# Performance work log

Hardware: AMD Instinct MI355X
Metric: run time of the kernel (lower is better)

The kernel has to match this reference:

```python
import jax, jax.numpy as jnp
import numpy as np

HEADS = 8
VTH = 1.0
TAU = 2.0          # spikingjelly LIFNode default tau
RS = 64            # region size for bi-level routing
TOPK = 4           # routed regions per query region
ALPHA = 2.0        # ATan surrogate alpha


@jax.custom_vjp
def spike(x):
    # Heaviside forward, ATan surrogate backward (spikingjelly surrogate.ATan)
    return (x >= 0.0).astype(x.dtype)

def _spike_fwd(x):
    return spike(x), x

def _spike_bwd(x, g):
    return (g * (ALPHA / 2.0) / (1.0 + (jnp.pi / 2.0 * ALPHA * x) ** 2),)

spike.defvjp(_spike_fwd, _spike_bwd)


def lif(x):
    # x: [Lt, b, L, dim]; multi-step LIF, v_reset=0 hard reset, detach_reset=True
    def step(v, xt):
        v = v + (xt - v) / TAU
        s = spike(v - VTH)
        v = v * (1.0 - jax.lax.stop_gradient(s))
        return v, s
    _, s = jax.lax.scan(step, jnp.zeros_like(x[0]), x)
    return s


def batchnorm(x, gamma, beta, eps=1e-5):
    # BatchNorm1d(dim) applied to [Lt*b, dim, L]: stats over (Lt, b, L) per channel
    mean = x.mean(axis=(0, 1, 2), keepdims=True)
    var = x.var(axis=(0, 1, 2), keepdims=True)
    return (x - mean) * jax.lax.rsqrt(var + eps) * gamma + beta


def bilevel_attn(s, Wqkv, bqkv, Wo, bo):
    Lt, b, L, dim = s.shape
    R = L // RS
    hd = dim // HEADS
    q, k, v = jnp.split(s @ Wqkv + bqkv, 3, axis=-1)            # each [Lt,b,L,dim]
    # coarse region-level routing on mean-pooled q/k
    qr = q.reshape(Lt, b, R, RS, dim).mean(3)                    # [Lt,b,R,dim]
    kr = k.reshape(Lt, b, R, RS, dim).mean(3)
    aff = jnp.einsum('tbrd,tbsd->tbrs', qr, kr)                  # [Lt,b,R,R]
    _, idx = jax.lax.top_k(aff, TOPK)                            # [Lt,b,R,TOPK]
    kreg = k.reshape(Lt, b, R, RS, HEADS, hd)
    vreg = v.reshape(Lt, b, R, RS, HEADS, hd)
    gidx = idx[:, :, :, :, None, None, None]
    kg = jnp.take_along_axis(kreg[:, :, None], gidx, axis=3).reshape(Lt, b, R, TOPK * RS, HEADS, hd)
    vg = jnp.take_along_axis(vreg[:, :, None], gidx, axis=3).reshape(Lt, b, R, TOPK * RS, HEADS, hd)
    qt = q.reshape(Lt, b, R, RS, HEADS, hd)
    scores = jnp.einsum('tbrihd,tbrjhd->tbrhij', qt, kg) / np.sqrt(hd).astype(np.float32)
    p = jax.nn.softmax(scores, axis=-1)
    out = jnp.einsum('tbrhij,tbrjhd->tbrihd', p, vg).reshape(Lt, b, L, dim)
    return out @ Wo + bo


def _block(x, bn1_gamma, bn1_beta, Wqkv, bqkv, Wo, bo,
           bn2_gamma, bn2_beta, W1, b1, W2, b2, scale):
    s1 = lif(batchnorm(x, bn1_gamma, bn1_beta))
    x = x + bilevel_attn(s1, Wqkv, bqkv, Wo, bo) * scale
    s2 = lif(batchnorm(x, bn2_gamma, bn2_beta))
    h = jax.nn.gelu(s2 @ W1 + b1, approximate=False)
    x = x + (h @ W2 + b2) * scale
    return x


def setup_inputs() -> dict:
    key = jax.random.key(0)
    ks = jax.random.split(key, 8)
    Lt, b, L, dim = 4, 8, 1024, 256
    x = jax.random.normal(ks[0], (Lt, b, L, dim), dtype=jnp.float32)
    w = lambda k, sh: 0.02 * jax.random.normal(k, sh, dtype=jnp.float32)
    return {
        'x': x,
        'bn1_gamma': jnp.ones((dim,), jnp.float32),
        'bn1_beta': jnp.zeros((dim,), jnp.float32),
        'Wqkv': w(ks[1], (dim, 3 * dim)),
        'bqkv': jnp.zeros((3 * dim,), jnp.float32),
        'Wo': w(ks[2], (dim, dim)),
        'bo': jnp.zeros((dim,), jnp.float32),
        'bn2_gamma': jnp.ones((dim,), jnp.float32),
        'bn2_beta': jnp.zeros((dim,), jnp.float32),
        'W1': w(ks[3], (dim, 4 * dim)),
        'b1': jnp.zeros((4 * dim,), jnp.float32),
        'W2': w(ks[4], (4 * dim, dim)),
        'b2': jnp.zeros((dim,), jnp.float32),
        'scale': jnp.array(0.5, jnp.float32),
        'Lt': Lt, 'b': b, 'L': L, 'dim': dim,
    }


def reference(x, bn1_gamma, bn1_beta, Wqkv, bqkv, Wo, bo,
              bn2_gamma, bn2_beta, W1, b1, W2, b2, scale,
              Lt, b, L, dim):
    return _block(x, bn1_gamma, bn1_beta, Wqkv, bqkv, Wo, bo,
                  bn2_gamma, bn2_beta, W1, b1, W2, b2, scale)
```

## Files before the change

kernel.cpp:

```cpp
#include <hip/hip_runtime.h>
#include <hip/hip_bf16.h>
#include <math.h>

typedef __hip_bfloat16 bf16;
typedef unsigned long long u64;
typedef unsigned int u32;

#define LTT 4
#define DIM 256
#define NTOK 32768
#define MT 2097152
#define NTOT 8388608

typedef __attribute__((ext_vector_type(8))) short short8;
typedef __attribute__((ext_vector_type(4))) float f32x4;
typedef __attribute__((ext_vector_type(4))) u32 u32x4;

__device__ __forceinline__ float ldin(const void* p, size_t i, int f) {
  float v = f ? ((const float*)p)[i] : __bfloat162float(((const bf16*)p)[i]);
  return isfinite(v) ? v : 0.0f;
}

__device__ __forceinline__ short bf16bits(float x) {
  union { bf16 b; short s; } u; u.b = __float2bfloat16(x); return u.s;
}

struct PtrPack { const void* p[14]; int n[14]; };

__global__ void probe_all_k(PtrPack pk, int* flags) {
  int b = blockIdx.x;
  int tid = threadIdx.x;
  const unsigned short* u = (const unsigned short*)pk.p[b];
  int nelem = pk.n[b];
  int n = nelem < 1024 ? nelem : 1024;
  bool big = false, nz = false;
  for (int i = tid; i < n; i += 64) {
    unsigned short h = u[i];
    if (((h >> 7) & 0xFF) >= 0xC0) big = true;
    if (h != 0) nz = true;
  }
  u64 bm = __ballot(big);
  u64 zm = __ballot(nz);
  if (tid == 0) {
    unsigned short h0 = u[0];
    int f = 0;
    if (bm != 0ull) f = 1;
    else if (h0 == 0 && (zm != 0ull || n == 1)) f = 1;
    flags[b] = f;
    if (b == 0) flags[15] = 1;
  }
}

__global__ void bnstats_k(const void* __restrict__ x, const int* __restrict__ fxp,
                          float* __restrict__ gsum, float* __restrict__ gsq) {
  int fx = *fxp;
  int c = threadIdx.x;
  int tok0 = blockIdx.x * 128;
  float s = 0.f, q = 0.f;
  for (int t = 0; t < 128; t++) {
    float v = ldin(x, (size_t)(tok0 + t) * DIM + c, fx);
    s += v; q += v * v;
  }
  atomicAdd(&gsum[c], s);
  atomicAdd(&gsq[c], q);
}

__global__ void lif_k(const void* __restrict__ x, const int* __restrict__ fxp,
                      const float* __restrict__ gsum, const float* __restrict__ gsq,
                      const void* __restrict__ gamma, const int* __restrict__ fgp,
                      const void* __restrict__ beta, const int* __restrict__ fbp,
                      u64* __restrict__ bits) {
  int fx = *fxp, fg = *fgp, fb = *fbp;
  int m = blockIdx.x * 256 + threadIdx.x;
  int c = m & (DIM - 1);
  int lane = threadIdx.x & 63;
  float mean = gsum[c] * (1.0f / 32768.0f);
  float var  = gsq[c] * (1.0f / 32768.0f) - mean * mean;
  float inv  = rsqrtf(var + 1e-5f);
  float g = ldin(gamma, c, fg), be = ldin(beta, c, fb);
  float v = 0.f;
  #pragma unroll
  for (int t = 0; t < LTT; t++) {
    size_t e = (size_t)t * MT + m;
    float xn = (ldin(x, e, fx) - mean) * inv * g + be;
    v = v + (xn - v) * 0.5f;
    bool sp = (v - 1.0f >= 0.0f);
    u64 bl = __ballot(sp);
    if (lane == 0) bits[e >> 6] = bl;
    v = sp ? 0.0f : v;
  }
}

__device__ __forceinline__ float gelu_f(float x) {
  return 0.5f * x * (1.0f + erff(x * 0.70710678118654752440f));
}

__global__ void wconv_all_k(const void* __restrict__ Wqkv, const void* __restrict__ Wo,
                            const void* __restrict__ W1, const void* __restrict__ W2,
                            const int* __restrict__ flags,
                            bf16* __restrict__ wqkvt, bf16* __restrict__ wot,
                            bf16* __restrict__ w1t, bf16* __restrict__ w2t) {
  int b = blockIdx.x, t = threadIdx.x;
  const void* W; const int* f; bf16* o; int K, N, n, kblk = 0;
  if (b < 768)       { W = Wqkv; f = flags + 3;  o = wqkvt; K = 256;  N = 768;  n = b; }
  else if (b < 1024) { W = Wo;   f = flags + 5;  o = wot;   K = 256;  N = 256;  n = b - 768; }
  else if (b < 2048) { W = W1;   f = flags + 9;  o = w1t;   K = 256;  N = 1024; n = b - 1024; }
  else { W = W2; f = flags + 11; o = w2t; K = 1024; N = 256;
         int q = b - 2048; kblk = q >> 8; n = q & 255; }
  int k = kblk * 256 + t;
  o[(size_t)n * K + k] = __float2bfloat16(ldin(W, (size_t)k * N + n, *f));
}

template <int MODE, int ABITS>
__global__ void __launch_bounds__(256)
dgemm_k(const void* __restrict__ Av, const bf16* __restrict__ Bt,
        const void* __restrict__ biasv, const int* __restrict__ fbp,
        void* O, const void* xinv, const int* __restrict__ fxp,
        const void* __restrict__ scalev, const int* __restrict__ fsp,
        int N, int K, size_t obase) {
  int tid = threadIdx.x;
  int lane = tid & 63, w = tid >> 6;
  int wr = w >> 1, wc = w & 1;
  int kq = lane >> 4, lr = lane & 15;
  int bm = blockIdx.y * 128, bn = blockIdx.x * 128;
  f32x4 acc[4][4] = {};

  if constexpr (ABITS) {
    __shared__ __align__(16) short lut[256][8];
    {
      short8 e;
      #pragma unroll
      for (int j = 0; j < 8; j++) e[j] = ((tid >> j) & 1) ? (short)0x3F80 : (short)0;
      *(short8*)&lut[tid][0] = e;
    }
    const u32* Abits = (const u32*)Av;
    u32 ab[4][8];
    #pragma unroll
    for (int i = 0; i < 4; i++) {
      const u32* rp = &Abits[(size_t)(bm + wr * 64 + i * 16 + lr) * 8];
      *(u32x4*)&ab[i][0] = *(const u32x4*)&rp[0];
      *(u32x4*)&ab[i][4] = *(const u32x4*)&rp[4];
    }
    __syncthreads();
    #pragma unroll
    for (int s = 0; s < 8; s++) {
      short8 af[4], bf[4];
      #pragma unroll
      for (int i = 0; i < 4; i++) {
        u32 byte = (ab[i][s] >> (kq * 8)) & 0xFFu;
        af[i] = *(const short8*)&lut[byte][0];
      }
      #pragma unroll
      for (int j = 0; j < 4; j++)
        bf[j] = *(const short8*)&Bt[(size_t)(bn + wc * 64 + j * 16 + lr) * 256 + s * 32 + kq * 8];
      #pragma unroll
      for (int i = 0; i < 4; i++)
        #pragma unroll
        for (int j = 0; j < 4; j++)
          acc[i][j] = __builtin_amdgcn_mfma_f32_16x16x32_bf16(af[i], bf[j], acc[i][j], 0, 0, 0);
    }
  } else {
    const bf16* Ab = (const bf16*)Av;
    for (int k0 = 0; k0 < K; k0 += 32) {
      short8 af[4], bf[4];
      #pragma unroll
      for (int i = 0; i < 4; i++)
        af[i] = *(const short8*)&Ab[(size_t)(bm + wr * 64 + i * 16 + lr) * K + k0 + kq * 8];
      #pragma unroll
      for (int j = 0; j < 4; j++)
        bf[j] = *(const short8*)&Bt[(size_t)(bn + wc * 64 + j * 16 + lr) * K + k0 + kq * 8];
      #pragma unroll
      for (int i = 0; i < 4; i++)
        #pragma unroll
        for (int j = 0; j < 4; j++)
          acc[i][j] = __builtin_amdgcn_mfma_f32_16x16x32_bf16(af[i], bf[j], acc[i][j], 0, 0, 0);
    }
  }

  float scl = 0.f;
  int fx = 0, fbias = *fbp;
  if (MODE == 4) { scl = ldin(scalev, 0, *fsp); fx = *fxp; }
  int row0 = bm + wr * 64 + kq * 4;
  int col0 = bn + wc * 64 + lr;
  #pragma unroll
  for (int j = 0; j < 4; j++) {
    int n = col0 + j * 16;
    float bb = ldin(biasv, n, fbias);
    #pragma unroll
    for (int i = 0; i < 4; i++) {
      #pragma unroll
      for (int r = 0; r < 4; r++) {
        int m = row0 + i * 16 + r;
        float v = acc[i][j][r] + bb;
        size_t o = obase + (size_t)m * N + n;
        if (MODE == 2) {
          ((bf16*)O)[o] = __float2bfloat16(gelu_f(v));
        } else if (MODE == 3) {
          ((bf16*)O)[o] = __float2bfloat16(v);
        } else {
          float base = ldin(xinv, o, fx);
          ((float*)O)[o] = base + scl * v;
        }
      }
    }
  }
}

__global__ void __launch_bounds__(256)
ffn_k(const u64* __restrict__ bits_, const bf16* __restrict__ w1t,
      const void* __restrict__ b1v, const int* __restrict__ f1p,
      const bf16* __restrict__ w2t,
      const void* __restrict__ b2v, const int* __restrict__ f2p,
      float* out, const void* __restrict__ scalev, const int* __restrict__ fsp) {
  __shared__ __align__(16) short lut[256][8];
  __shared__ __align__(16) short hlds[16][64][8];
  int tid = threadIdx.x;
  int lane = tid & 63, w = tid >> 6;
  int kq = lane >> 4, lr = lane & 15;
  int m0 = blockIdx.x * 64;
  {
    short8 e;
    #pragma unroll
    for (int j = 0; j < 8; j++) e[j] = ((tid >> j) & 1) ? (short)0x3F80 : (short)0;
    *(short8*)&lut[tid][0] = e;
  }
  const u32* Abits = (const u32*)bits_;
  u32 ab[4][8];
  #pragma unroll
  for (int i = 0; i < 4; i++) {
    const u32* rp = &Abits[(size_t)(m0 + i * 16 + lr) * 8];
    *(u32x4*)&ab[i][0] = *(const u32x4*)&rp[0];
    *(u32x4*)&ab[i][4] = *(const u32x4*)&rp[4];
  }
  int f1 = *f1p;
  f32x4 acc2[4][4] = {};
  __syncthreads();

  for (int c = 0; c < 8; c++) {
    f32x4 accA[4][2] = {};
    #pragma unroll
    for (int s = 0; s < 8; s++) {
      short8 af[4], bf2[2];
      #pragma unroll
      for (int i = 0; i < 4; i++) {
        u32 byte = (ab[i][s] >> (kq * 8)) & 0xFFu;
        af[i] = *(const short8*)&lut[byte][0];
      }
      #pragma unroll
      for (int j = 0; j < 2; j++)
        bf2[j] = *(const short8*)&w1t[(size_t)(c * 128 + w * 32 + j * 16 + lr) * 256 + s * 32 + kq * 8];
      #pragma unroll
      for (int i = 0; i < 4; i++)
        #pragma unroll
        for (int j = 0; j < 2; j++)
          accA[i][j] = __builtin_amdgcn_mfma_f32_16x16x32_bf16(af[i], bf2[j], accA[i][j], 0, 0, 0);
    }
    #pragma unroll
    for (int j = 0; j < 2; j++) {
      int cl = w * 32 + j * 16 + lr;
      float bb = ldin(b1v, c * 128 + cl, f1);
      #pragma unroll
      for (int i = 0; i < 4; i++)
        #pragma unroll
        for (int r = 0; r < 4; r++) {
          int row = i * 16 + kq * 4 + r;
          hlds[cl >> 3][row][cl & 7] = bf16bits(gelu_f(accA[i][j][r] + bb));
        }
    }
    __syncthreads();
    #pragma unroll
    for (int ks = 0; ks < 4; ks++) {
      short8 af[4], bf4[4];
      #pragma unroll
      for (int i = 0; i < 4; i++)
        af[i] = *(const short8*)&hlds[ks * 4 + kq][i * 16 + lr][0];
      #pragma unroll
      for (int j = 0; j < 4; j++)
        bf4[j] = *(const short8*)&w2t[(size_t)(w * 64 + j * 16 + lr) * 1024 + c * 128 + ks * 32 + kq * 8];
      #pragma unroll
      for (int i = 0; i < 4; i++)
        #pragma unroll
        for (int j = 0; j < 4; j++)
          acc2[i][j] = __builtin_amdgcn_mfma_f32_16x16x32_bf16(af[i], bf4[j], acc2[i][j], 0, 0, 0);
    }
    __syncthreads();
  }

  float scl = ldin(scalev, 0, *fsp);
  int f2 = *f2p;
  #pragma unroll
  for (int j = 0; j < 4; j++) {
    int n = w * 64 + j * 16 + lr;
    float bb = ldin(b2v, n, f2);
    #pragma unroll
    for (int i = 0; i < 4; i++)
      #pragma unroll
      for (int r = 0; r < 4; r++) {
        int row = m0 + i * 16 + kq * 4 + r;
        size_t o = (size_t)row * 256 + n;
        out[o] = out[o] + scl * (acc2[i][j][r] + bb);
      }
  }
}

__global__ void regmean_k(const u64* __restrict__ bits, float* __restrict__ sreg) {
  int blk = blockIdx.x;
  int c = threadIdx.x;
  float s = 0.f;
  for (int i = 0; i < 64; i++) {
    u64 w = bits[(size_t)(blk * 64 + i) * 4 + (c >> 6)];
    s += (float)((w >> (c & 63)) & 1ull);
  }
  sreg[(size_t)blk * 256 + c] = s * (1.0f / 64.0f);
}

__global__ void __launch_bounds__(256)
pgemm_k(const float* __restrict__ A,
        const void* __restrict__ Bv, const int* __restrict__ fBp,
        const void* __restrict__ biasv, const int* __restrict__ fbp,
        float* __restrict__ Oq) {
  int fB = *fBp, fb = *fbp;
  __shared__ float Ast[16][68];
  __shared__ float Bs[16][68];
  int tid = threadIdx.x;
  int bm = blockIdx.y * 64, bn = blockIdx.x * 64;
  int tr = tid >> 4, tc = tid & 15;
  float acc[4][4] = {};
  for (int k0 = 0; k0 < 256; k0 += 16) {
    for (int t = tid; t < 1024; t += 256) {
      int m = t >> 4, k = t & 15;
      Ast[k][m] = A[(size_t)(bm + m) * 256 + k0 + k];
    }
    for (int t = tid; t < 1024; t += 256) {
      int k = t >> 6, n = t & 63;
      Bs[k][n] = ldin(Bv, (size_t)(k0 + k) * 768 + bn + n, fB);
    }
    __syncthreads();
    #pragma unroll
    for (int kk = 0; kk < 16; kk++) {
      float4 a4 = *(const float4*)&Ast[kk][tr * 4];
      float4 b4 = *(const float4*)&Bs[kk][tc * 4];
      float a[4] = {a4.x, a4.y, a4.z, a4.w};
      float b[4] = {b4.x, b4.y, b4.z, b4.w};
      #pragma unroll
      for (int i = 0; i < 4; i++)
        #pragma unroll
        for (int jj = 0; jj < 4; jj++)
          acc[i][jj] += a[i] * b[jj];
    }
    __syncthreads();
  }
  #pragma unroll
  for (int i = 0; i < 4; i++)
    #pragma unroll
    for (int jj = 0; jj < 4; jj++) {
      int n = bn + tc * 4 + jj;
      Oq[(size_t)(bm + tr * 4 + i) * 512 + n] = acc[i][jj] + ldin(biasv, n, fb);
    }
}

__global__ void afftopk_k(const float* __restrict__ qkr, int* __restrict__ idx) {
  int blk = blockIdx.x;
  int tb = blk >> 4;
  int tid = threadIdx.x;
  int s_ = tid >> 4, p = tid & 15;
  __shared__ float part[256];
  __shared__ float aff[16];
  const float* qrow = qkr + (size_t)blk * 512;
  const float* krow = qkr + (size_t)(tb * 16 + s_) * 512 + 256;
  float acc = 0.f;
  for (int c = p * 16; c < p * 16 + 16; c++) acc += qrow[c] * krow[c];
  part[tid] = acc;
  __syncthreads();
  if (tid < 16) {
    float a = 0.f;
    for (int pp = 0; pp < 16; pp++) a += part[tid * 16 + pp];
    aff[tid] = a;
  }
  __syncthreads();
  if (tid == 0) {
    bool taken[16] = {};
    for (int kk = 0; kk < 4; kk++) {
      float best = -INFINITY; int bi = 0;
      for (int i = 0; i < 16; i++)
        if (!taken[i] && aff[i] > best) { best = aff[i]; bi = i; }
      taken[bi] = true;
      idx[blk * 4 + kk] = bi;
    }
  }
}

__global__ void __launch_bounds__(256)
attn_k(const bf16* __restrict__ qkv, const int* __restrict__ idx,
       bf16* __restrict__ ctx) {
  __shared__ __align__(16) short Ks[256][32];
  __shared__ __align__(16) short Vs[32][256];
  __shared__ __align__(16) short Ps[4][16][256];
  int blk = blockIdx.x;
  int h = blk & 7, br = blk >> 3;
  int b = br >> 4;
  int tid = threadIdx.x;
  int base = br * 64;
  int r0 = idx[br * 4 + 0], r1 = idx[br * 4 + 1];
  int r2 = idx[br * 4 + 2], r3 = idx[br * 4 + 3];

  #pragma unroll
  for (int c = 0; c < 4; c++) {
    int g = c * 256 + tid;
    int tk = g >> 2, ch = g & 3;
    int rs = tk >> 6;
    int rid = (rs & 2) ? ((rs & 1) ? r3 : r2) : ((rs & 1) ? r1 : r0);
    int gt = b * 1024 + rid * 64 + (tk & 63);
    short8 v = *(const short8*)&qkv[(size_t)gt * 768 + 256 + h * 32 + ch * 8];
    *(short8*)&Ks[tk][ch * 8] = v;
  }
  {
    int tk = tid;
    int rs = tk >> 6;
    int rid = (rs & 2) ? ((rs & 1) ? r3 : r2) : ((rs & 1) ? r1 : r0);
    int gt = b * 1024 + rid * 64 + (tk & 63);
    const bf16* vp = &qkv[(size_t)gt * 768 + 512 + h * 32];
    short vv[32];
    *(short8*)&vv[0]  = *(const short8*)&vp[0];
    *(short8*)&vv[8]  = *(const short8*)&vp[8];
    *(short8*)&vv[16] = *(const short8*)&vp[16];
    *(short8*)&vv[24] = *(const short8*)&vp[24];
    #pragma unroll
    for (int d = 0; d < 32; d++)
      Vs[d][(tk + 8 * d) & 255] = vv[d];
  }
  __syncthreads();

  int w = tid >> 6, lane = tid & 63, kq = lane >> 4, lr = lane & 15;

  short8 qf = *(const short8*)&qkv[(size_t)(base + w * 16 + lr) * 768 + h * 32 + kq * 8];

  f32x4 s[16];
  #pragma unroll
  for (int nt = 0; nt < 16; nt++) {
    short8 kf = *(const short8*)&Ks[nt * 16 + lr][kq * 8];
    f32x4 z = {0.f, 0.f, 0.f, 0.f};
    s[nt] = __builtin_amdgcn_mfma_f32_16x16x32_bf16(qf, kf, z, 0, 0, 0);
  }

  const float cs = 0.17677669529663687f;
  float mx[4] = {-INFINITY, -INFINITY, -INFINITY, -INFINITY};
  #pragma unroll
  for (int nt = 0; nt < 16; nt++)
    #pragma unroll
    for (int r = 0; r < 4; r++) mx[r] = fmaxf(mx[r], s[nt][r]);
  #pragma unroll
  for (int m = 1; m < 16; m <<= 1)
    #pragma unroll
    for (int r = 0; r < 4; r++) mx[r] = fmaxf(mx[r], __shfl_xor(mx[r], m, 64));
  float sum[4] = {0.f, 0.f, 0.f, 0.f};
  #pragma unroll
  for (int nt = 0; nt < 16; nt++)
    #pragma unroll
    for (int r = 0; r < 4; r++) {
      float e = __expf((s[nt][r] - mx[r]) * cs);
      s[nt][r] = e; sum[r] += e;
    }
  #pragma unroll
  for (int m = 1; m < 16; m <<= 1)
    #pragma unroll
    for (int r = 0; r < 4; r++) sum[r] += __shfl_xor(sum[r], m, 64);
  float inv[4];
  #pragma unroll
  for (int r = 0; r < 4; r++) inv[r] = 1.0f / sum[r];

  #pragma unroll
  for (int nt = 0; nt < 16; nt++)
    #pragma unroll
    for (int r = 0; r < 4; r++) {
      int row = kq * 4 + r;
      int col = nt * 16 + lr;
      Ps[w][row][col ^ ((row & 7) << 3)] = bf16bits(s[nt][r] * inv[r]);
    }
  __syncthreads();

  f32x4 o0 = {0.f, 0.f, 0.f, 0.f}, o1 = {0.f, 0.f, 0.f, 0.f};
  #pragma unroll
  for (int kc = 0; kc < 8; kc++) {
    short8 pf = *(const short8*)
        &Ps[w][lr][(kc ^ ((lr >> 2) & 1)) * 32 + (kq ^ (lr & 3)) * 8];
    int d0 = lr, d1 = 16 + lr;
    short8 vf0 = *(const short8*)&Vs[d0][(kc * 32 + kq * 8 + 8 * d0) & 255];
    short8 vf1 = *(const short8*)&Vs[d1][(kc * 32 + kq * 8 + 8 * d1) & 255];
    o0 = __builtin_amdgcn_mfma_f32_16x16x32_bf16(pf, vf0, o0, 0, 0, 0);
    o1 = __builtin_amdgcn_mfma_f32_16x16x32_bf16(pf, vf1, o1, 0, 0, 0);
  }

  #pragma unroll
  for (int r = 0; r < 4; r++) {
    int q = base + w * 16 + kq * 4 + r;
    ctx[(size_t)q * 256 + h * 32 + lr]      = __float2bfloat16(o0[r]);
    ctx[(size_t)q * 256 + h * 32 + 16 + lr] = __float2bfloat16(o1[r]);
  }
}

extern "C" void kernel_launch(void* const* d_in, const int* in_sizes, int n_in,
                              void* d_out, int out_size, void* d_ws, size_t ws_size,
                              hipStream_t stream) {
  const void* x_in = d_in[0];
  const void* Wqkv = d_in[3];
  const void* bqkv = d_in[4];
  const void* Wo   = d_in[5];
  const void* bo   = d_in[6];
  const void* W1   = d_in[9];
  const void* b1   = d_in[10];
  const void* W2   = d_in[11];
  const void* b2   = d_in[12];
  const void* scale = d_in[13];

  const size_t MISC = 256 + 1048576 + 524288 + 8192 + 1048576 + 2048
                    + 393216 + 131072 + 524288 + 524288;
  int C;
  if      (MISC + (size_t)32 * 2097152 <= ws_size) C = 32;
  else if (MISC + (size_t)8  * 2097152 <= ws_size) C = 8;
  else if (MISC + (size_t)4  * 2097152 <= ws_size) C = 4;
  else                                             C = 1;
  size_t r0 = (size_t)C * 2097152;

  char* ws = (char*)d_ws;
  int*  flags = (int*)ws;
  char* p = ws + 256;
  bf16* qkvb = (bf16*)p;
  bf16* ctxb = (bf16*)(p + (size_t)C * 1572864);
  p += r0;
  float* qkr  = (float*)p;  p += 1048576;
  float* sreg = (float*)p;  p += 524288;
  int*   idxb = (int*)p;    p += 8192;
  u64*   bits = (u64*)p;    p += 1048576;
  float* gsum = (float*)p;  p += 2048;
  float* gsq  = gsum + 256;
  bf16* wqkvt = (bf16*)p;   p += 393216;
  bf16* wot   = (bf16*)p;   p += 131072;
  bf16* w1t   = (bf16*)p;   p += 524288;
  bf16* w2t   = (bf16*)p;   p += 524288;
  float* out  = (float*)d_out;
  const int* F14 = flags + 14;

  hipMemsetAsync(flags, 0, 256, stream);
  PtrPack pk;
  for (int i = 0; i < 14; i++) { pk.p[i] = d_in[i]; pk.n[i] = in_sizes[i]; }
  probe_all_k<<<14, 64, 0, stream>>>(pk, flags);

  wconv_all_k<<<3072, 256, 0, stream>>>(Wqkv, Wo, W1, W2, flags,
                                        wqkvt, wot, w1t, w2t);

  hipMemsetAsync(gsum, 0, 512 * sizeof(float), stream);
  bnstats_k<<<256, 256, 0, stream>>>(x_in, flags + 0, gsum, gsq);
  lif_k<<<MT / 256, 256, 0, stream>>>(x_in, flags + 0, gsum, gsq,
                                      d_in[1], flags + 1, d_in[2], flags + 2, bits);

  regmean_k<<<512, 256, 0, stream>>>(bits, sreg);
  pgemm_k<<<dim3(8, 8), 256, 0, stream>>>(sreg, Wqkv, flags + 3, bqkv, flags + 4, qkr);
  afftopk_k<<<512, 256, 0, stream>>>(qkr, idxb);

  for (int gb = 0; gb < 32; gb += C) {
    size_t tok0 = (size_t)gb * 1024;
    dgemm_k<3, 1><<<dim3(6, C * 8), 256, 0, stream>>>(
        (const void*)((const u32*)bits + tok0 * 8), wqkvt,
        bqkv, flags + 4, qkvb, nullptr, F14, nullptr, F14, 768, 256, 0);
    attn_k<<<C * 128, 256, 0, stream>>>(qkvb, idxb + gb * 64, ctxb);
    dgemm_k<4, 0><<<dim3(2, C * 8), 256, 0, stream>>>(
        ctxb, wot, bo, flags + 6, out, x_in, flags + 0,
        scale, flags + 13, 256, 256, tok0 * 256);
  }

  hipMemsetAsync(gsum, 0, 512 * sizeof(float), stream);
  bnstats_k<<<256, 256, 0, stream>>>(out, flags + 15, gsum, gsq);
  lif_k<<<MT / 256, 256, 0, stream>>>(out, flags + 15, gsum, gsq,
                                      d_in[7], flags + 7, d_in[8], flags + 8, bits);

  ffn_k<<<NTOK / 64, 256, 0, stream>>>(bits, w1t, b1, flags + 10,
                                       w2t, b2, flags + 12,
                                       out, scale, flags + 13);
}
```

Before: 487.0 us.

## Widen FFN kernel to 512 threads and stage expanded spike tile in LDS

The fused FFN kernel now runs 8 waves per 64-row block instead of 4, with each wave owning half as many output columns in both GEMMs. The spike bits for the block are expanded once through the LUT into a shared A tile, replacing per-wave register bit unpacking. This aims to raise occupancy and latency hiding on the MFMA loops at the cost of more LDS (about 32KB for the A tile) and an extra barrier per chunk. A 16-chunk fallback for the attention workspace is also added.

```diff
diff --git a/kernel.cpp b/kernel.cpp
--- a/kernel.cpp
+++ b/kernel.cpp
@@ -206,91 +206,79 @@
   }
 }
 
-__global__ void __launch_bounds__(256)
+__global__ void __launch_bounds__(512)
 ffn_k(const u64* __restrict__ bits_, const bf16* __restrict__ w1t,
       const void* __restrict__ b1v, const int* __restrict__ f1p,
       const bf16* __restrict__ w2t,
       const void* __restrict__ b2v, const int* __restrict__ f2p,
       float* out, const void* __restrict__ scalev, const int* __restrict__ fsp) {
   __shared__ __align__(16) short lut[256][8];
+  __shared__ __align__(16) short As[32][64][8];
   __shared__ __align__(16) short hlds[16][64][8];
   int tid = threadIdx.x;
   int lane = tid & 63, w = tid >> 6;
   int kq = lane >> 4, lr = lane & 15;
   int m0 = blockIdx.x * 64;
-  {
+  if (tid < 256) {
     short8 e;
     #pragma unroll
     for (int j = 0; j < 8; j++) e[j] = ((tid >> j) & 1) ? (short)0x3F80 : (short)0;
     *(short8*)&lut[tid][0] = e;
   }
-  const u32* Abits = (const u32*)bits_;
-  u32 ab[4][8];
-  #pragma unroll
-  for (int i = 0; i < 4; i++) {
-    const u32* rp = &Abits[(size_t)(m0 + i * 16 + lr) * 8];
-    *(u32x4*)&ab[i][0] = *(const u32x4*)&rp[0];
-    *(u32x4*)&ab[i][4] = *(const u32x4*)&rp[4];
+  __syncthreads();
+  {
+    int row = tid >> 3, word = tid & 7;
+    u32 val = ((const u32*)bits_)[(size_t)(m0 + row) * 8 + word];
+    #pragma unroll
+    for (int q = 0; q < 4; q++) {
+      u32 byte = (val >> (q * 8)) & 0xFFu;
+      *(short8*)&As[word * 4 + q][row][0] = *(const short8*)&lut[byte][0];
+    }
   }
   int f1 = *f1p;
-  f32x4 acc2[4][4] = {};
+  f32x4 acc2[4][2] = {};
   __syncthreads();
 
   for (int c = 0; c < 8; c++) {
-    f32x4 accA[4][2] = {};
+    f32x4 accA[4] = {};
     #pragma unroll
     for (int s = 0; s < 8; s++) {
-      short8 af[4], bf2[2];
+      short8 bfw = *(const short8*)&w1t[(size_t)(c * 128 + w * 16 + lr) * 256 + s * 32 + kq * 8];
       #pragma unroll
       for (int i = 0; i < 4; i++) {
-        u32 byte = (ab[i][s] >> (kq * 8)) & 0xFFu;
-        af[i] = *(const short8*)&lut[byte][0];
+        short8 af = *(const short8*)&As[s * 4 + kq][i * 16 + lr][0];
+        accA[i] = __builtin_amdgcn_mfma_f32_16x16x32_bf16(af, bfw, accA[i], 0, 0, 0);
       }
-      #pragma unroll
-      for (int j = 0; j < 2; j++)
-        bf2[j] = *(const short8*)&w1t[(size_t)(c * 128 + w * 32 + j * 16 + lr) * 256 + s * 32 + kq * 8];
+    }
+    __syncthreads();
+    {
+      int cl = w * 16 + lr;
+      float bb = ldin(b1v, c * 128 + cl, f1);
       #pragma unroll
       for (int i = 0; i < 4; i++)
         #pragma unroll
-        for (int j = 0; j < 2; j++)
-          accA[i][j] = __builtin_amdgcn_mfma_f32_16x16x32_bf16(af[i], bf2[j], accA[i][j], 0, 0, 0);
-    }
-    #pragma unroll
-    for (int j = 0; j < 2; j++) {
-      int cl = w * 32 + j * 16 + lr;
-      float bb = ldin(b1v, c * 128 + cl, f1);
-      #pragma unroll
-      for (int i = 0; i < 4; i++)
-        #pragma unroll
-        for (int r = 0; r < 4; r++) {
-          int row = i * 16 + kq * 4 + r;
-          hlds[cl >> 3][row][cl & 7] = bf16bits(gelu_f(accA[i][j][r] + bb));
-        }
+        for (int r = 0; r < 4; r++)
+          hlds[cl >> 3][i * 16 + kq * 4 + r][cl & 7] = bf16bits(gelu_f(accA[i][r] + bb));
     }
     __syncthreads();
     #pragma unroll
     for (int ks = 0; ks < 4; ks++) {
-      short8 af[4], bf4[4];
-      #pragma unroll
-      for (int i = 0; i < 4; i++)
-        af[i] = *(const short8*)&hlds[ks * 4 + kq][i * 16 + lr][0];
-      #pragma unroll
-      for (int j = 0; j < 4; j++)
-        bf4[j] = *(const short8*)&w2t[(size_t)(w * 64 + j * 16 + lr) * 1024 + c * 128 + ks * 32 + kq * 8];
-      #pragma unroll
-      for (int i = 0; i < 4; i++)
-        #pragma unroll
-        for (int j = 0; j < 4; j++)
-          acc2[i][j] = __builtin_amdgcn_mfma_f32_16x16x32_bf16(af[i], bf4[j], acc2[i][j], 0, 0, 0);
-    }
-    __syncthreads();
+      short8 bf0 = *(const short8*)&w2t[(size_t)(w * 32 + lr) * 1024 + c * 128 + ks * 32 + kq * 8];
+      short8 bf1 = *(const short8*)&w2t[(size_t)(w * 32 + 16 + lr) * 1024 + c * 128 + ks * 32 + kq * 8];
+      #pragma unroll
+      for (int i = 0; i < 4; i++) {
+        short8 af = *(const short8*)&hlds[ks * 4 + kq][i * 16 + lr][0];
+        acc2[i][0] = __builtin_amdgcn_mfma_f32_16x16x32_bf16(af, bf0, acc2[i][0], 0, 0, 0);
+        acc2[i][1] = __builtin_amdgcn_mfma_f32_16x16x32_bf16(af, bf1, acc2[i][1], 0, 0, 0);
+      }
+    }
   }
 
   float scl = ldin(scalev, 0, *fsp);
   int f2 = *f2p;
   #pragma unroll
-  for (int j = 0; j < 4; j++) {
-    int n = w * 64 + j * 16 + lr;
+  for (int j = 0; j < 2; j++) {
+    int n = w * 32 + j * 16 + lr;
     float bb = ldin(b2v, n, f2);
     #pragma unroll
     for (int i = 0; i < 4; i++)
@@ -517,6 +505,7 @@
                     + 393216 + 131072 + 524288 + 524288;
   int C;
   if      (MISC + (size_t)32 * 2097152 <= ws_size) C = 32;
+  else if (MISC + (size_t)16 * 2097152 <= ws_size) C = 16;
   else if (MISC + (size_t)8  * 2097152 <= ws_size) C = 8;
   else if (MISC + (size_t)4  * 2097152 <= ws_size) C = 4;
   else                                             C = 1;
@@ -574,7 +563,7 @@
   lif_k<<<MT / 256, 256, 0, stream>>>(out, flags + 15, gsum, gsq,
                                       d_in[7], flags + 7, d_in[8], flags + 8, bits);
 
-  ffn_k<<<NTOK / 64, 256, 0, stream>>>(bits, w1t, b1, flags + 10,
+  ffn_k<<<NTOK / 64, 512, 0, stream>>>(bits, w1t, b1, flags + 10,
                                        w2t, b2, flags + 12,
                                        out, scale, flags + 13);
 }
```

Result: faster. 440.4 us (-9.6%).
